# Optimization experiments

Hardware: AMD Instinct MI355X
Metric: run time of the kernel (lower is better)

Reference implementation:

```python
import jax, jax.numpy as jnp
import numpy as np

B, DIM, Hs, Ws = 2, 64, 48, 48
HEADS, DIM_HEAD = 4, 16
INNER = HEADS * DIM_HEAD  # 64
MLP_DIM = 256


def setup_inputs() -> dict:
    key = jax.random.key(0)
    ks = jax.random.split(key, 10)
    w = lambda k, shape: (jax.random.normal(k, shape, jnp.float32) * 0.02)
    return dict(
        x=jax.random.normal(ks[0], (B, DIM, Hs, Ws), jnp.float32),
        y=jax.random.normal(ks[1], (B, DIM, Hs, Ws), jnp.float32),
        ln1_g=jnp.ones((DIM,), jnp.float32), ln1_b=jnp.zeros((DIM,), jnp.float32),
        w_sa1=w(ks[2], (DIM, INNER)), w_sa2=w(ks[3], (DIM, INNER)),
        w_se1=w(ks[4], (DIM, INNER)), w_se2=w(ks[5], (DIM, INNER)),
        w_out=w(ks[6], (INNER, DIM)), b_out=jnp.zeros((DIM,), jnp.float32),
        ln2_g=jnp.ones((DIM,), jnp.float32), ln2_b=jnp.zeros((DIM,), jnp.float32),
        w1=w(ks[7], (DIM, MLP_DIM)), b1=jnp.zeros((MLP_DIM,), jnp.float32),
        w2=w(ks[8], (MLP_DIM, DIM)), b2=jnp.zeros((DIM,), jnp.float32),
    )


def _layer_norm(t, g, b, eps=1e-5):
    m = t.mean(-1, keepdims=True)
    v = t.var(-1, keepdims=True)
    return (t - m) * jax.lax.rsqrt(v + eps) * g + b


def reference(x, y, ln1_g, ln1_b, w_sa1, w_sa2, w_se1, w_se2, w_out, b_out,
              ln2_g, ln2_b, w1, b1, w2, b2):
    b, c, h, wdt = x.shape
    xt = x.reshape(b, c, h * wdt).transpose(0, 2, 1)  # B n C
    yt = y.reshape(b, c, h * wdt).transpose(0, 2, 1)
    n = xt.shape[1]
    scale = DIM_HEAD ** (-0.5)

    # PreNorm: same LayerNorm applied to both x and y (shared params)
    xn = _layer_norm(xt, ln1_g, ln1_b)
    yn = _layer_norm(yt, ln1_g, ln1_b)

    def split_heads(t, wm):  # B n C -> B h n d
        return (t @ wm).reshape(b, n, HEADS, DIM_HEAD).transpose(0, 2, 1, 3)

    y1 = split_heads(yn, w_sa1)
    y2 = split_heads(yn, w_sa2)
    x1 = split_heads(xn, w_se1)
    x2 = split_heads(xn, w_se2)

    # spatial attention map: n x n from y branch
    sacm = jax.nn.softmax(jnp.einsum('bhid,bhjd->bhij', y1, y2) * scale, axis=-1)
    # channel attention map: d x d from x branch
    secm = jax.nn.softmax(jnp.einsum('bhni,bhnj->bhij', x1, x2) * scale / (n / DIM_HEAD), axis=-1)

    out1 = jnp.einsum('bhij,bhjd->bhid', sacm, x1)  # spatial map applied to x values
    out2 = jnp.einsum('bhni,bhij->bhnj', y1, secm)  # channel map applied to y values
    out = (out1 * out2).transpose(0, 2, 1, 3).reshape(b, n, INNER)
    xt = xt + out @ w_out + b_out  # residual around attention

    # MLP with PreNorm + residual, LeakyReLU slope 0.01 (torch default)
    xn2 = _layer_norm(xt, ln2_g, ln2_b)
    hid = jax.nn.leaky_relu(xn2 @ w1 + b1, negative_slope=0.01)
    xt = xt + hid @ w2 + b2

    return xt.transpose(0, 2, 1).reshape(b, c, h, wdt)
```

## Files before the change

### kernel.cpp

```cpp
#include <hip/hip_runtime.h>

#define HW 2304
#define CH 64
typedef unsigned short ushort_t;
typedef __attribute__((ext_vector_type(8))) short bf16x8;
typedef __attribute__((ext_vector_type(4))) float f32x4;

#define QSCL (0.25f * 1.44269504088896340736f)
#define SECM_SCL (0.25f / 144.f)
#define MFMA(a, b, c) __builtin_amdgcn_mfma_f32_16x16x32_bf16((a), (b), (c), 0, 0, 0)

static __device__ __forceinline__ ushort_t f2bf(float f) {
    union { float f; unsigned u; } v; v.f = f;
    unsigned r = v.u + 0x7FFFu + ((v.u >> 16) & 1u);
    return (ushort_t)(r >> 16);
}
static __device__ __forceinline__ unsigned cvtpk(float a, float b) {
    unsigned r;
    asm("v_cvt_pk_bf16_f32 %0, %1, %2" : "=v"(r) : "v"(a), "v"(b));
    return r;
}
union U8 { unsigned u[4]; bf16x8 v; };

__global__ __launch_bounds__(256) void k_wconv(
    const float* __restrict__ wsa1, const float* __restrict__ wsa2,
    const float* __restrict__ wse1, const float* __restrict__ wse2,
    const float* __restrict__ w_out, const float* __restrict__ w1,
    const float* __restrict__ w2,
    ushort_t* __restrict__ wsa1T, ushort_t* __restrict__ wsa2T,
    ushort_t* __restrict__ wse1T, ushort_t* __restrict__ wse2T,
    ushort_t* __restrict__ w_outT, ushort_t* __restrict__ wT1, ushort_t* __restrict__ wT2,
    float* __restrict__ sacc)
{
    const int blk = blockIdx.x, tid = threadIdx.x;
    if (blk < 8) sacc[blk * 256 + tid] = 0.f;
    if (blk < 80) {
        const int mi = blk >> 4;
        const float* s = mi == 0 ? wsa1 : mi == 1 ? wsa2 : mi == 2 ? wse1 : mi == 3 ? wse2 : w_out;
        ushort_t* d = mi == 0 ? wsa1T : mi == 1 ? wsa2T : mi == 2 ? wse1T : mi == 3 ? wse2T : w_outT;
        const int o = (blk & 15) * 256 + tid;
        d[o] = f2bf(s[(o & 63) * 64 + (o >> 6)]);
    } else if (blk < 144) {
        const int o = (blk - 80) * 256 + tid;
        wT1[o] = f2bf(w1[(o & 63) * 256 + (o >> 6)]);
    } else {
        const int o = (blk - 144) * 256 + tid;
        wT2[o] = f2bf(w2[(o & 255) * 64 + (o >> 8)]);
    }
}

__global__ __launch_bounds__(64) void k_ln_proj(
    const float* __restrict__ x, const float* __restrict__ y,
    const float* __restrict__ g, const float* __restrict__ bb,
    const ushort_t* __restrict__ wsa1T, const ushort_t* __restrict__ wsa2T,
    const ushort_t* __restrict__ wse1T, const ushort_t* __restrict__ wse2T,
    float* __restrict__ y1f, ushort_t* __restrict__ qbf, ushort_t* __restrict__ kbf,
    ushort_t* __restrict__ vtbf, float* __restrict__ sacc)
{
    __shared__ ushort_t ldsA[16 * 24 + 32];
    __shared__ ushort_t ldsB[16 * 24 + 32];
    const int task = blockIdx.x;
    const int jt = blockIdx.y;
    const int rt = task % 144;
    const int b  = (task / 144) & 1;
    const int branch = task / 288;
    const int lane = threadIdx.x;
    const int r = lane & 15, cg = lane >> 4;
    const int q0 = rt * 16;
    const float* in = (branch ? y : x) + (size_t)b * CH * HW + q0 + r;
    float lo[8], hi[8];
    float s = 0.f, sq = 0.f;
    #pragma unroll
    for (int ki = 0; ki < 8; ++ki) {
        lo[ki] = in[(size_t)(8 * cg + ki) * HW];
        hi[ki] = in[(size_t)(32 + 8 * cg + ki) * HW];
        s += lo[ki] + hi[ki];
        sq += lo[ki] * lo[ki] + hi[ki] * hi[ki];
    }
    s  += __shfl_xor(s, 16);  s  += __shfl_xor(s, 32);
    sq += __shfl_xor(sq, 16); sq += __shfl_xor(sq, 32);
    const float m  = s * (1.f / 64.f);
    const float rs = rsqrtf(sq * (1.f / 64.f) - m * m + 1e-5f);
    float ga[16], be[16];
    {
        const float4* gp = (const float4*)g;
        const float4* bp = (const float4*)bb;
        *(float4*)&ga[0]  = gp[2 * cg];     *(float4*)&ga[4]  = gp[2 * cg + 1];
        *(float4*)&ga[8]  = gp[8 + 2 * cg]; *(float4*)&ga[12] = gp[9 + 2 * cg];
        *(float4*)&be[0]  = bp[2 * cg];     *(float4*)&be[4]  = bp[2 * cg + 1];
        *(float4*)&be[8]  = bp[8 + 2 * cg]; *(float4*)&be[12] = bp[9 + 2 * cg];
    }
    float nlo[8], nhi[8];
    #pragma unroll
    for (int ki = 0; ki < 8; ++ki) {
        nlo[ki] = (lo[ki] - m) * rs * ga[ki]     + be[ki];
        nhi[ki] = (hi[ki] - m) * rs * ga[8 + ki] + be[8 + ki];
    }
    U8 alo, ahi;
    #pragma unroll
    for (int p = 0; p < 4; ++p) {
        alo.u[p] = cvtpk(nlo[2 * p], nlo[2 * p + 1]);
        ahi.u[p] = cvtpk(nhi[2 * p], nhi[2 * p + 1]);
    }
    const ushort_t* wp1 = branch ? wsa1T : wse1T;
    const ushort_t* wp2 = branch ? wsa2T : wse2T;
    const f32x4 zero4 = {0.f, 0.f, 0.f, 0.f};
    const int bh = b * 4 + jt;
    bf16x8 bl1 = *(const bf16x8*)(wp1 + (jt * 16 + r) * 64 + 8 * cg);
    bf16x8 bh1 = *(const bf16x8*)(wp1 + (jt * 16 + r) * 64 + 32 + 8 * cg);
    f32x4 acc1 = zero4;
    acc1 = MFMA(alo.v, bl1, acc1);
    acc1 = MFMA(ahi.v, bh1, acc1);
    bf16x8 bl2 = *(const bf16x8*)(wp2 + (jt * 16 + r) * 64 + 8 * cg);
    bf16x8 bh2 = *(const bf16x8*)(wp2 + (jt * 16 + r) * 64 + 32 + 8 * cg);
    f32x4 acc2 = zero4;
    acc2 = MFMA(alo.v, bl2, acc2);
    acc2 = MFMA(ahi.v, bh2, acc2);
    if (branch == 0) {
        uint2 pk1; pk1.x = cvtpk(acc1[0], acc1[1]); pk1.y = cvtpk(acc1[2], acc1[3]);
        *(uint2*)(vtbf + (size_t)(bh * 16 + r) * HW + q0 + 4 * cg) = pk1;
        *(uint2*)&ldsA[r * 24 + 4 * cg] = pk1;
        uint2 pk2; pk2.x = cvtpk(acc2[0], acc2[1]); pk2.y = cvtpk(acc2[2], acc2[3]);
        *(uint2*)&ldsB[r * 24 + 4 * cg] = pk2;
        bf16x8 af = {0, 0, 0, 0, 0, 0, 0, 0};
        bf16x8 bf_ = {0, 0, 0, 0, 0, 0, 0, 0};
        if (cg < 2) {
            af  = *(const bf16x8*)&ldsA[r * 24 + 8 * cg];
            bf_ = *(const bf16x8*)&ldsB[r * 24 + 8 * cg];
        }
        f32x4 sp = MFMA(af, bf_, zero4);
        #pragma unroll
        for (int ri = 0; ri < 4; ++ri)
            atomicAdd(&sacc[bh * 256 + (4 * cg + ri) * 16 + r], sp[ri]);
    } else {
        #pragma unroll
        for (int ri = 0; ri < 4; ++ri) {
            const int q = q0 + 4 * cg + ri;
            y1f[((size_t)bh * HW + q) * 16 + r] = acc1[ri];
            qbf[((size_t)bh * HW + q) * 16 + r] = f2bf(acc1[ri] * QSCL);
            kbf[((size_t)bh * HW + q) * 16 + r] = f2bf(acc2[ri]);
        }
    }
}

__global__ __launch_bounds__(512) void k_attn(
    const ushort_t* __restrict__ qbf, const ushort_t* __restrict__ kbf,
    const ushort_t* __restrict__ vtbf, const float* __restrict__ y1f,
    const float* __restrict__ sacc, ushort_t* __restrict__ obf)
{
    __shared__ uint4 pbuf4[8][80];
    __shared__ f32x4 cacc[8][64];
    __shared__ float clsum[8][64];
    __shared__ float sraw[256];
    __shared__ float smv[256];
    const int qt = blockIdx.x, bh = blockIdx.y;
    const int tid = threadIdx.x;
    const int w = tid >> 6, lane = tid & 63;
    const int q16 = lane & 15, g = lane >> 4;
    const int q0 = qt * 16;
    if (tid < 256) sraw[tid] = sacc[bh * 256 + tid] * SECM_SCL;
    __syncthreads();
    if (tid < 256) {
        const int i = tid >> 4;
        float mx = -1e30f;
        #pragma unroll
        for (int jj = 0; jj < 16; ++jj) mx = fmaxf(mx, sraw[i * 16 + jj]);
        float sum = 0.f;
        #pragma unroll
        for (int jj = 0; jj < 16; ++jj) sum += __expf(sraw[i * 16 + jj] - mx);
        smv[tid] = __expf(sraw[tid] - mx) / sum;
    }

    bf16x8 qfrag = {0, 0, 0, 0, 0, 0, 0, 0};
    if (g < 2) qfrag = *(const bf16x8*)(qbf + ((size_t)bh * HW + q0 + q16) * 16 + g * 8);

    unsigned char* pw = (unsigned char*)&pbuf4[w][0];
    const ushort_t* kbase = kbf + (size_t)bh * HW * 16;
    const ushort_t* vbase = vtbf + (size_t)(bh * 16 + q16) * HW;
    f32x4 oacc = {0.f, 0.f, 0.f, 0.f};
    float lsum = 0.f;
    const f32x4 zero4 = {0.f, 0.f, 0.f, 0.f};

    #pragma unroll 3
    for (int wi = 0; wi < 9; ++wi) {
        const int k0 = w * 288 + wi * 32;
        bf16x8 kf0 = *(const bf16x8*)(kbase + (size_t)(k0 + q16) * 16 + (g & 1) * 8);
        bf16x8 kf1 = *(const bf16x8*)(kbase + (size_t)(k0 + 16 + q16) * 16 + (g & 1) * 8);
        f32x4 s0 = MFMA(kf0, qfrag, zero4);
        f32x4 s1 = MFMA(kf1, qfrag, zero4);
        const float e00 = exp2f(s0[0]), e01 = exp2f(s0[1]), e02 = exp2f(s0[2]), e03 = exp2f(s0[3]);
        const float e10 = exp2f(s1[0]), e11 = exp2f(s1[1]), e12 = exp2f(s1[2]), e13 = exp2f(s1[3]);
        lsum += ((e00 + e01) + (e02 + e03)) + ((e10 + e11) + (e12 + e13));
        *(unsigned*)(pw + q16 * 80 + 8 * g)      = cvtpk(e00, e01);
        *(unsigned*)(pw + q16 * 80 + 8 * g + 4)  = cvtpk(e02, e03);
        *(unsigned*)(pw + q16 * 80 + 32 + 8 * g) = cvtpk(e10, e11);
        *(unsigned*)(pw + q16 * 80 + 36 + 8 * g) = cvtpk(e12, e13);
        bf16x8 vfrag = *(const bf16x8*)(vbase + k0 + 8 * g);
        bf16x8 pfrag = *(const bf16x8*)(pw + q16 * 80 + 16 * g);
        oacc = MFMA(vfrag, pfrag, oacc);
    }
    cacc[w][lane] = oacc;
    clsum[w][lane] = lsum;
    __syncthreads();
    if (tid < 64) {
        f32x4 t = cacc[0][lane];
        float L = clsum[0][lane];
        #pragma unroll
        for (int ww = 1; ww < 8; ++ww) {
            f32x4 tw = cacc[ww][lane];
            t[0] += tw[0]; t[1] += tw[1]; t[2] += tw[2]; t[3] += tw[3];
            L += clsum[ww][lane];
        }
        L += __shfl_xor(L, 16);
        L += __shfl_xor(L, 32);
        const float invl = 1.f / L;
        const float* yrow = y1f + ((size_t)bh * HW + q0 + q16) * 16;
        float ya[16];
        #pragma unroll
        for (int i = 0; i < 4; ++i) *(float4*)&ya[4 * i] = ((const float4*)yrow)[i];
        float gate[4] = {0.f, 0.f, 0.f, 0.f};
        #pragma unroll
        for (int i = 0; i < 16; ++i) {
            #pragma unroll
            for (int rr = 0; rr < 4; ++rr) gate[rr] += ya[i] * smv[i * 16 + g * 4 + rr];
        }
        const int b = bh >> 2, h = bh & 3;
        float r0 = t[0] * invl * gate[0];
        float r1 = t[1] * invl * gate[1];
        float r2 = t[2] * invl * gate[2];
        float r3 = t[3] * invl * gate[3];
        uint2 pk; pk.x = cvtpk(r0, r1); pk.y = cvtpk(r2, r3);
        *(uint2*)(obf + ((size_t)b * HW + q0 + q16) * 64 + h * 16 + g * 4) = pk;
    }
}

__global__ __launch_bounds__(256) void k_tail(
    const ushort_t* __restrict__ obf, const float* __restrict__ x,
    const ushort_t* __restrict__ w_outT, const float* __restrict__ b_out,
    const float* __restrict__ g2, const float* __restrict__ bt2,
    const ushort_t* __restrict__ wT1, const float* __restrict__ b1,
    const ushort_t* __restrict__ wT2, const float* __restrict__ b2,
    float* __restrict__ out)
{
    __shared__ float xtile[16][68];
    __shared__ ushort_t hh[16 * 264 + 16];
    const int t = blockIdx.x;
    const int b = t / 144;
    const int q0 = (t % 144) * 16;
    const int tid = threadIdx.x;
    const int w = tid >> 6, lane = tid & 63;
    const int r = lane & 15, cg = lane >> 4;
    const f32x4 zero4 = {0.f, 0.f, 0.f, 0.f};
    const ushort_t* arow = obf + ((size_t)b * HW + q0 + r) * 64;
    bf16x8 alo = *(const bf16x8*)(arow + 8 * cg);
    bf16x8 ahi = *(const bf16x8*)(arow + 32 + 8 * cg);
    {
        bf16x8 bl = *(const bf16x8*)(w_outT + (w * 16 + r) * 64 + 8 * cg);
        bf16x8 bh_ = *(const bf16x8*)(w_outT + (w * 16 + r) * 64 + 32 + 8 * cg);
        f32x4 acc = zero4;
        acc = MFMA(alo, bl, acc);
        acc = MFMA(ahi, bh_, acc);
        const int c = w * 16 + r;
        const float bo = b_out[c];
        float4 xr = *(const float4*)(x + (size_t)b * CH * HW + (size_t)c * HW + q0 + 4 * cg);
        xtile[4 * cg + 0][c] = acc[0] + bo + xr.x;
        xtile[4 * cg + 1][c] = acc[1] + bo + xr.y;
        xtile[4 * cg + 2][c] = acc[2] + bo + xr.z;
        xtile[4 * cg + 3][c] = acc[3] + bo + xr.w;
    }
    __syncthreads();
    float s = 0.f, sq = 0.f;
    #pragma unroll
    for (int j = 0; j < 16; ++j) {
        const float v = xtile[r][cg * 16 + j];
        s += v; sq += v * v;
    }
    s  += __shfl_xor(s, 16);  s  += __shfl_xor(s, 32);
    sq += __shfl_xor(sq, 16); sq += __shfl_xor(sq, 32);
    const float m  = s * (1.f / 64.f);
    const float rs = rsqrtf(sq * (1.f / 64.f) - m * m + 1e-5f);
    float ga[16], be[16];
    {
        const float4* gp = (const float4*)g2;
        const float4* bp = (const float4*)bt2;
        *(float4*)&ga[0]  = gp[2 * cg];     *(float4*)&ga[4]  = gp[2 * cg + 1];
        *(float4*)&ga[8]  = gp[8 + 2 * cg]; *(float4*)&ga[12] = gp[9 + 2 * cg];
        *(float4*)&be[0]  = bp[2 * cg];     *(float4*)&be[4]  = bp[2 * cg + 1];
        *(float4*)&be[8]  = bp[8 + 2 * cg]; *(float4*)&be[12] = bp[9 + 2 * cg];
    }
    float nlo[8], nhi[8];
    #pragma unroll
    for (int ki = 0; ki < 8; ++ki) {
        nlo[ki] = (xtile[r][8 * cg + ki]      - m) * rs * ga[ki]     + be[ki];
        nhi[ki] = (xtile[r][32 + 8 * cg + ki] - m) * rs * ga[8 + ki] + be[8 + ki];
    }
    U8 axlo, axhi;
    #pragma unroll
    for (int p = 0; p < 4; ++p) {
        axlo.u[p] = cvtpk(nlo[2 * p], nlo[2 * p + 1]);
        axhi.u[p] = cvtpk(nhi[2 * p], nhi[2 * p + 1]);
    }
    #pragma unroll
    for (int jj = 0; jj < 4; ++jj) {
        const int jt = 4 * w + jj;
        bf16x8 bl = *(const bf16x8*)(wT1 + (jt * 16 + r) * 64 + 8 * cg);
        bf16x8 bh_ = *(const bf16x8*)(wT1 + (jt * 16 + r) * 64 + 32 + 8 * cg);
        f32x4 acc = zero4;
        acc = MFMA(axlo.v, bl, acc);
        acc = MFMA(axhi.v, bh_, acc);
        const int c = jt * 16 + r;
        const float bias = b1[c];
        #pragma unroll
        for (int ri = 0; ri < 4; ++ri) {
            float vv = acc[ri] + bias;
            vv = fmaxf(vv, 0.01f * vv);
            hh[(4 * cg + ri) * 264 + c] = f2bf(vv);
        }
    }
    __syncthreads();
    bf16x8 ha[8];
    #pragma unroll
    for (int kw = 0; kw < 8; ++kw)
        ha[kw] = *(const bf16x8*)&hh[r * 264 + kw * 32 + 8 * cg];
    f32x4 acc = zero4;
    #pragma unroll
    for (int kw = 0; kw < 8; ++kw) {
        bf16x8 bf_ = *(const bf16x8*)(wT2 + (w * 16 + r) * 256 + kw * 32 + 8 * cg);
        acc = MFMA(ha[kw], bf_, acc);
    }
    const int c = w * 16 + r;
    const float bias = b2[c];
    float4 res;
    res.x = acc[0] + bias + xtile[4 * cg + 0][c];
    res.y = acc[1] + bias + xtile[4 * cg + 1][c];
    res.z = acc[2] + bias + xtile[4 * cg + 2][c];
    res.w = acc[3] + bias + xtile[4 * cg + 3][c];
    *(float4*)(out + (size_t)b * CH * HW + (size_t)c * HW + q0 + 4 * cg) = res;
}

extern "C" void kernel_launch(void* const* d_in, const int* in_sizes, int n_in,
                              void* d_out, int out_size, void* d_ws, size_t ws_size,
                              hipStream_t stream)
{
    (void)in_sizes; (void)n_in; (void)out_size; (void)ws_size;
    const float* x     = (const float*)d_in[0];
    const float* y     = (const float*)d_in[1];
    const float* ln1_g = (const float*)d_in[2];
    const float* ln1_b = (const float*)d_in[3];
    const float* w_sa1 = (const float*)d_in[4];
    const float* w_sa2 = (const float*)d_in[5];
    const float* w_se1 = (const float*)d_in[6];
    const float* w_se2 = (const float*)d_in[7];
    const float* w_out = (const float*)d_in[8];
    const float* b_out = (const float*)d_in[9];
    const float* ln2_g = (const float*)d_in[10];
    const float* ln2_b = (const float*)d_in[11];
    const float* w1    = (const float*)d_in[12];
    const float* b1    = (const float*)d_in[13];
    const float* w2    = (const float*)d_in[14];
    const float* b2    = (const float*)d_in[15];
    float* out = (float*)d_out;

    const size_t NP = 8ull * HW * 16;
    float* p = (float*)d_ws;
    float* y1f  = p;  p += NP;
    float* sacc = p;  p += 2048;
    ushort_t* u = (ushort_t*)p;
    ushort_t* qbf   = u;  u += NP;
    ushort_t* kbf   = u;  u += NP;
    ushort_t* vtbf  = u;  u += NP;
    ushort_t* obf   = u;  u += NP;
    ushort_t* wsa1T = u;  u += 4096;
    ushort_t* wsa2T = u;  u += 4096;
    ushort_t* wse1T = u;  u += 4096;
    ushort_t* wse2T = u;  u += 4096;
    ushort_t* w_outT= u;  u += 4096;
    ushort_t* wT1   = u;  u += 16384;
    ushort_t* wT2   = u;  u += 16384;

    k_wconv<<<208, 256, 0, stream>>>(w_sa1, w_sa2, w_se1, w_se2, w_out, w1, w2,
                                     wsa1T, wsa2T, wse1T, wse2T, w_outT, wT1, wT2,
                                     sacc);
    k_ln_proj<<<dim3(576, 4), 64, 0, stream>>>(x, y, ln1_g, ln1_b,
                                               wsa1T, wsa2T, wse1T, wse2T,
                                               y1f, qbf, kbf, vtbf, sacc);
    k_attn<<<dim3(144, 8), 512, 0, stream>>>(qbf, kbf, vtbf, y1f, sacc, obf);
    k_tail<<<288, 256, 0, stream>>>(obf, x, w_outT, b_out, ln2_g, ln2_b,
                                    wT1, b1, wT2, b2, out);
}
```

Measured before the change: 119.3 us.

## Fuse all stages into one persistent kernel with software grid barriers

Replaces the four separate launches (weight conversion, LN+projection, attention, tail MLP) with a small init kernel plus one persistent kernel of 768 blocks that runs each stage in turn, separated by atomic-counter grid barriers. Stages share a union of LDS buffers, and work is redistributed across 256-thread blocks, with the attention stage using 4 waves instead of 8. The aim is to remove per-launch overhead and the gaps between dependent kernels. In exchange it relies on all 768 blocks being co-resident (launch bounds request 3 blocks per CU), which risks deadlock or spin overhead. The attention parallelism per block is also reduced.

```diff
diff --git a/kernel.cpp b/kernel.cpp
--- a/kernel.cpp
+++ b/kernel.cpp
@@ -2,6 +2,7 @@
 
 #define HW 2304
 #define CH 64
+#define NBLK 768
 typedef unsigned short ushort_t;
 typedef __attribute__((ext_vector_type(8))) short bf16x8;
 typedef __attribute__((ext_vector_type(4))) float f32x4;
@@ -22,320 +23,337 @@
 }
 union U8 { unsigned u[4]; bf16x8 v; };
 
-__global__ __launch_bounds__(256) void k_wconv(
+__global__ __launch_bounds__(256) void k_init(int* __restrict__ bar, float* __restrict__ sacc)
+{
+    const int tid = threadIdx.x;
+    if (tid < 16) bar[tid] = 0;
+    #pragma unroll
+    for (int i = 0; i < 8; ++i) sacc[i * 256 + tid] = 0.f;
+}
+
+static __device__ __forceinline__ void gridbar(int* bar, int phase)
+{
+    __syncthreads();
+    if (threadIdx.x == 0) {
+        int prev = __hip_atomic_fetch_add(&bar[0], 1, __ATOMIC_ACQ_REL, __HIP_MEMORY_SCOPE_AGENT);
+        if (prev == NBLK - 1) {
+            __hip_atomic_store(&bar[0], 0, __ATOMIC_RELAXED, __HIP_MEMORY_SCOPE_AGENT);
+            __hip_atomic_store(&bar[1], phase, __ATOMIC_RELEASE, __HIP_MEMORY_SCOPE_AGENT);
+        } else {
+            while (__hip_atomic_load(&bar[1], __ATOMIC_ACQUIRE, __HIP_MEMORY_SCOPE_AGENT) < phase)
+                __builtin_amdgcn_s_sleep(1);
+        }
+    }
+    __syncthreads();
+}
+
+__global__ __launch_bounds__(256, 3) void k_mega(
+    const float* __restrict__ x, const float* __restrict__ y,
+    const float* __restrict__ ln1g, const float* __restrict__ ln1b,
     const float* __restrict__ wsa1, const float* __restrict__ wsa2,
     const float* __restrict__ wse1, const float* __restrict__ wse2,
-    const float* __restrict__ w_out, const float* __restrict__ w1,
-    const float* __restrict__ w2,
+    const float* __restrict__ w_out, const float* __restrict__ b_out,
+    const float* __restrict__ ln2g, const float* __restrict__ ln2b,
+    const float* __restrict__ w1, const float* __restrict__ mb1,
+    const float* __restrict__ w2, const float* __restrict__ mb2,
+    float* __restrict__ y1f, float* __restrict__ sacc, int* __restrict__ bar,
+    ushort_t* __restrict__ qbf, ushort_t* __restrict__ kbf,
+    ushort_t* __restrict__ vtbf, ushort_t* __restrict__ obf,
     ushort_t* __restrict__ wsa1T, ushort_t* __restrict__ wsa2T,
     ushort_t* __restrict__ wse1T, ushort_t* __restrict__ wse2T,
     ushort_t* __restrict__ w_outT, ushort_t* __restrict__ wT1, ushort_t* __restrict__ wT2,
-    float* __restrict__ sacc)
-{
-    const int blk = blockIdx.x, tid = threadIdx.x;
-    if (blk < 8) sacc[blk * 256 + tid] = 0.f;
-    if (blk < 80) {
-        const int mi = blk >> 4;
-        const float* s = mi == 0 ? wsa1 : mi == 1 ? wsa2 : mi == 2 ? wse1 : mi == 3 ? wse2 : w_out;
-        ushort_t* d = mi == 0 ? wsa1T : mi == 1 ? wsa2T : mi == 2 ? wse1T : mi == 3 ? wse2T : w_outT;
-        const int o = (blk & 15) * 256 + tid;
-        d[o] = f2bf(s[(o & 63) * 64 + (o >> 6)]);
-    } else if (blk < 144) {
-        const int o = (blk - 80) * 256 + tid;
-        wT1[o] = f2bf(w1[(o & 63) * 256 + (o >> 6)]);
-    } else {
-        const int o = (blk - 144) * 256 + tid;
-        wT2[o] = f2bf(w2[(o & 255) * 64 + (o >> 8)]);
-    }
-}
-
-__global__ __launch_bounds__(64) void k_ln_proj(
-    const float* __restrict__ x, const float* __restrict__ y,
-    const float* __restrict__ g, const float* __restrict__ bb,
-    const ushort_t* __restrict__ wsa1T, const ushort_t* __restrict__ wsa2T,
-    const ushort_t* __restrict__ wse1T, const ushort_t* __restrict__ wse2T,
-    float* __restrict__ y1f, ushort_t* __restrict__ qbf, ushort_t* __restrict__ kbf,
-    ushort_t* __restrict__ vtbf, float* __restrict__ sacc)
-{
-    __shared__ ushort_t ldsA[16 * 24 + 32];
-    __shared__ ushort_t ldsB[16 * 24 + 32];
-    const int task = blockIdx.x;
-    const int jt = blockIdx.y;
-    const int rt = task % 144;
-    const int b  = (task / 144) & 1;
-    const int branch = task / 288;
-    const int lane = threadIdx.x;
-    const int r = lane & 15, cg = lane >> 4;
-    const int q0 = rt * 16;
-    const float* in = (branch ? y : x) + (size_t)b * CH * HW + q0 + r;
-    float lo[8], hi[8];
-    float s = 0.f, sq = 0.f;
-    #pragma unroll
-    for (int ki = 0; ki < 8; ++ki) {
-        lo[ki] = in[(size_t)(8 * cg + ki) * HW];
-        hi[ki] = in[(size_t)(32 + 8 * cg + ki) * HW];
-        s += lo[ki] + hi[ki];
-        sq += lo[ki] * lo[ki] + hi[ki] * hi[ki];
-    }
-    s  += __shfl_xor(s, 16);  s  += __shfl_xor(s, 32);
-    sq += __shfl_xor(sq, 16); sq += __shfl_xor(sq, 32);
-    const float m  = s * (1.f / 64.f);
-    const float rs = rsqrtf(sq * (1.f / 64.f) - m * m + 1e-5f);
-    float ga[16], be[16];
-    {
-        const float4* gp = (const float4*)g;
-        const float4* bp = (const float4*)bb;
-        *(float4*)&ga[0]  = gp[2 * cg];     *(float4*)&ga[4]  = gp[2 * cg + 1];
-        *(float4*)&ga[8]  = gp[8 + 2 * cg]; *(float4*)&ga[12] = gp[9 + 2 * cg];
-        *(float4*)&be[0]  = bp[2 * cg];     *(float4*)&be[4]  = bp[2 * cg + 1];
-        *(float4*)&be[8]  = bp[8 + 2 * cg]; *(float4*)&be[12] = bp[9 + 2 * cg];
-    }
-    float nlo[8], nhi[8];
-    #pragma unroll
-    for (int ki = 0; ki < 8; ++ki) {
-        nlo[ki] = (lo[ki] - m) * rs * ga[ki]     + be[ki];
-        nhi[ki] = (hi[ki] - m) * rs * ga[8 + ki] + be[8 + ki];
-    }
-    U8 alo, ahi;
-    #pragma unroll
-    for (int p = 0; p < 4; ++p) {
-        alo.u[p] = cvtpk(nlo[2 * p], nlo[2 * p + 1]);
-        ahi.u[p] = cvtpk(nhi[2 * p], nhi[2 * p + 1]);
-    }
-    const ushort_t* wp1 = branch ? wsa1T : wse1T;
-    const ushort_t* wp2 = branch ? wsa2T : wse2T;
-    const f32x4 zero4 = {0.f, 0.f, 0.f, 0.f};
-    const int bh = b * 4 + jt;
-    bf16x8 bl1 = *(const bf16x8*)(wp1 + (jt * 16 + r) * 64 + 8 * cg);
-    bf16x8 bh1 = *(const bf16x8*)(wp1 + (jt * 16 + r) * 64 + 32 + 8 * cg);
-    f32x4 acc1 = zero4;
-    acc1 = MFMA(alo.v, bl1, acc1);
-    acc1 = MFMA(ahi.v, bh1, acc1);
-    bf16x8 bl2 = *(const bf16x8*)(wp2 + (jt * 16 + r) * 64 + 8 * cg);
-    bf16x8 bh2 = *(const bf16x8*)(wp2 + (jt * 16 + r) * 64 + 32 + 8 * cg);
-    f32x4 acc2 = zero4;
-    acc2 = MFMA(alo.v, bl2, acc2);
-    acc2 = MFMA(ahi.v, bh2, acc2);
-    if (branch == 0) {
-        uint2 pk1; pk1.x = cvtpk(acc1[0], acc1[1]); pk1.y = cvtpk(acc1[2], acc1[3]);
-        *(uint2*)(vtbf + (size_t)(bh * 16 + r) * HW + q0 + 4 * cg) = pk1;
-        *(uint2*)&ldsA[r * 24 + 4 * cg] = pk1;
-        uint2 pk2; pk2.x = cvtpk(acc2[0], acc2[1]); pk2.y = cvtpk(acc2[2], acc2[3]);
-        *(uint2*)&ldsB[r * 24 + 4 * cg] = pk2;
-        bf16x8 af = {0, 0, 0, 0, 0, 0, 0, 0};
-        bf16x8 bf_ = {0, 0, 0, 0, 0, 0, 0, 0};
-        if (cg < 2) {
-            af  = *(const bf16x8*)&ldsA[r * 24 + 8 * cg];
-            bf_ = *(const bf16x8*)&ldsB[r * 24 + 8 * cg];
-        }
-        f32x4 sp = MFMA(af, bf_, zero4);
-        #pragma unroll
-        for (int ri = 0; ri < 4; ++ri)
-            atomicAdd(&sacc[bh * 256 + (4 * cg + ri) * 16 + r], sp[ri]);
-    } else {
-        #pragma unroll
-        for (int ri = 0; ri < 4; ++ri) {
-            const int q = q0 + 4 * cg + ri;
-            y1f[((size_t)bh * HW + q) * 16 + r] = acc1[ri];
-            qbf[((size_t)bh * HW + q) * 16 + r] = f2bf(acc1[ri] * QSCL);
-            kbf[((size_t)bh * HW + q) * 16 + r] = f2bf(acc2[ri]);
-        }
-    }
-}
-
-__global__ __launch_bounds__(512) void k_attn(
-    const ushort_t* __restrict__ qbf, const ushort_t* __restrict__ kbf,
-    const ushort_t* __restrict__ vtbf, const float* __restrict__ y1f,
-    const float* __restrict__ sacc, ushort_t* __restrict__ obf)
-{
-    __shared__ uint4 pbuf4[8][80];
-    __shared__ f32x4 cacc[8][64];
-    __shared__ float clsum[8][64];
-    __shared__ float sraw[256];
-    __shared__ float smv[256];
-    const int qt = blockIdx.x, bh = blockIdx.y;
-    const int tid = threadIdx.x;
-    const int w = tid >> 6, lane = tid & 63;
-    const int q16 = lane & 15, g = lane >> 4;
-    const int q0 = qt * 16;
-    if (tid < 256) sraw[tid] = sacc[bh * 256 + tid] * SECM_SCL;
-    __syncthreads();
-    if (tid < 256) {
-        const int i = tid >> 4;
-        float mx = -1e30f;
-        #pragma unroll
-        for (int jj = 0; jj < 16; ++jj) mx = fmaxf(mx, sraw[i * 16 + jj]);
-        float sum = 0.f;
-        #pragma unroll
-        for (int jj = 0; jj < 16; ++jj) sum += __expf(sraw[i * 16 + jj] - mx);
-        smv[tid] = __expf(sraw[tid] - mx) / sum;
-    }
-
-    bf16x8 qfrag = {0, 0, 0, 0, 0, 0, 0, 0};
-    if (g < 2) qfrag = *(const bf16x8*)(qbf + ((size_t)bh * HW + q0 + q16) * 16 + g * 8);
-
-    unsigned char* pw = (unsigned char*)&pbuf4[w][0];
-    const ushort_t* kbase = kbf + (size_t)bh * HW * 16;
-    const ushort_t* vbase = vtbf + (size_t)(bh * 16 + q16) * HW;
-    f32x4 oacc = {0.f, 0.f, 0.f, 0.f};
-    float lsum = 0.f;
-    const f32x4 zero4 = {0.f, 0.f, 0.f, 0.f};
-
-    #pragma unroll 3
-    for (int wi = 0; wi < 9; ++wi) {
-        const int k0 = w * 288 + wi * 32;
-        bf16x8 kf0 = *(const bf16x8*)(kbase + (size_t)(k0 + q16) * 16 + (g & 1) * 8);
-        bf16x8 kf1 = *(const bf16x8*)(kbase + (size_t)(k0 + 16 + q16) * 16 + (g & 1) * 8);
-        f32x4 s0 = MFMA(kf0, qfrag, zero4);
-        f32x4 s1 = MFMA(kf1, qfrag, zero4);
-        const float e00 = exp2f(s0[0]), e01 = exp2f(s0[1]), e02 = exp2f(s0[2]), e03 = exp2f(s0[3]);
-        const float e10 = exp2f(s1[0]), e11 = exp2f(s1[1]), e12 = exp2f(s1[2]), e13 = exp2f(s1[3]);
-        lsum += ((e00 + e01) + (e02 + e03)) + ((e10 + e11) + (e12 + e13));
-        *(unsigned*)(pw + q16 * 80 + 8 * g)      = cvtpk(e00, e01);
-        *(unsigned*)(pw + q16 * 80 + 8 * g + 4)  = cvtpk(e02, e03);
-        *(unsigned*)(pw + q16 * 80 + 32 + 8 * g) = cvtpk(e10, e11);
-        *(unsigned*)(pw + q16 * 80 + 36 + 8 * g) = cvtpk(e12, e13);
-        bf16x8 vfrag = *(const bf16x8*)(vbase + k0 + 8 * g);
-        bf16x8 pfrag = *(const bf16x8*)(pw + q16 * 80 + 16 * g);
-        oacc = MFMA(vfrag, pfrag, oacc);
-    }
-    cacc[w][lane] = oacc;
-    clsum[w][lane] = lsum;
-    __syncthreads();
-    if (tid < 64) {
-        f32x4 t = cacc[0][lane];
-        float L = clsum[0][lane];
-        #pragma unroll
-        for (int ww = 1; ww < 8; ++ww) {
-            f32x4 tw = cacc[ww][lane];
-            t[0] += tw[0]; t[1] += tw[1]; t[2] += tw[2]; t[3] += tw[3];
-            L += clsum[ww][lane];
-        }
-        L += __shfl_xor(L, 16);
-        L += __shfl_xor(L, 32);
-        const float invl = 1.f / L;
-        const float* yrow = y1f + ((size_t)bh * HW + q0 + q16) * 16;
-        float ya[16];
-        #pragma unroll
-        for (int i = 0; i < 4; ++i) *(float4*)&ya[4 * i] = ((const float4*)yrow)[i];
-        float gate[4] = {0.f, 0.f, 0.f, 0.f};
-        #pragma unroll
-        for (int i = 0; i < 16; ++i) {
-            #pragma unroll
-            for (int rr = 0; rr < 4; ++rr) gate[rr] += ya[i] * smv[i * 16 + g * 4 + rr];
-        }
-        const int b = bh >> 2, h = bh & 3;
-        float r0 = t[0] * invl * gate[0];
-        float r1 = t[1] * invl * gate[1];
-        float r2 = t[2] * invl * gate[2];
-        float r3 = t[3] * invl * gate[3];
-        uint2 pk; pk.x = cvtpk(r0, r1); pk.y = cvtpk(r2, r3);
-        *(uint2*)(obf + ((size_t)b * HW + q0 + q16) * 64 + h * 16 + g * 4) = pk;
-    }
-}
-
-__global__ __launch_bounds__(256) void k_tail(
-    const ushort_t* __restrict__ obf, const float* __restrict__ x,
-    const ushort_t* __restrict__ w_outT, const float* __restrict__ b_out,
-    const float* __restrict__ g2, const float* __restrict__ bt2,
-    const ushort_t* __restrict__ wT1, const float* __restrict__ b1,
-    const ushort_t* __restrict__ wT2, const float* __restrict__ b2,
     float* __restrict__ out)
 {
-    __shared__ float xtile[16][68];
-    __shared__ ushort_t hh[16 * 264 + 16];
-    const int t = blockIdx.x;
-    const int b = t / 144;
-    const int q0 = (t % 144) * 16;
-    const int tid = threadIdx.x;
-    const int w = tid >> 6, lane = tid & 63;
-    const int r = lane & 15, cg = lane >> 4;
+    union SM {
+        struct { uint4 pbuf4[4][80]; f32x4 cacc[4][64]; float clsum[4][64];
+                 float sraw[256]; float smv[256]; } a;
+        struct { float xtile[16][68]; ushort_t hh[16 * 264 + 16]; } t;
+        struct { ushort_t A[4][416]; ushort_t B[4][416]; } l;
+    };
+    __shared__ SM sm;
     const f32x4 zero4 = {0.f, 0.f, 0.f, 0.f};
-    const ushort_t* arow = obf + ((size_t)b * HW + q0 + r) * 64;
-    bf16x8 alo = *(const bf16x8*)(arow + 8 * cg);
-    bf16x8 ahi = *(const bf16x8*)(arow + 32 + 8 * cg);
+
     {
-        bf16x8 bl = *(const bf16x8*)(w_outT + (w * 16 + r) * 64 + 8 * cg);
-        bf16x8 bh_ = *(const bf16x8*)(w_outT + (w * 16 + r) * 64 + 32 + 8 * cg);
+        const int idx = blockIdx.x * 256 + threadIdx.x;
+        if (idx < 20480) {
+            const int mi = idx >> 12, o = idx & 4095;
+            const float* s = mi == 0 ? wsa1 : mi == 1 ? wsa2 : mi == 2 ? wse1 : mi == 3 ? wse2 : w_out;
+            ushort_t* d = mi == 0 ? wsa1T : mi == 1 ? wsa2T : mi == 2 ? wse1T : mi == 3 ? wse2T : w_outT;
+            d[o] = f2bf(s[(o & 63) * 64 + (o >> 6)]);
+        } else if (idx < 36864) {
+            const int o = idx - 20480;
+            wT1[o] = f2bf(w1[(o & 63) * 256 + (o >> 6)]);
+        } else if (idx < 53248) {
+            const int o = idx - 36864;
+            wT2[o] = f2bf(w2[(o & 255) * 64 + (o >> 8)]);
+        }
+    }
+    gridbar(bar, 1);
+
+    {
+        const int tid = threadIdx.x;
+        const int w = tid >> 6, lane = tid & 63;
+        const int task = blockIdx.x + w * NBLK;
+        if (task < 2304) {
+            const int jt = task / 576;
+            const int t576 = task % 576;
+            const int rt = t576 % 144;
+            const int b  = (t576 / 144) & 1;
+            const int branch = t576 / 288;
+            const int r = lane & 15, cg = lane >> 4;
+            const int q0 = rt * 16;
+            const float* xin = (branch ? y : x) + (size_t)b * CH * HW + q0 + r;
+            float lo[8], hi[8];
+            float s = 0.f, sq = 0.f;
+            #pragma unroll
+            for (int ki = 0; ki < 8; ++ki) {
+                lo[ki] = xin[(size_t)(8 * cg + ki) * HW];
+                hi[ki] = xin[(size_t)(32 + 8 * cg + ki) * HW];
+                s += lo[ki] + hi[ki];
+                sq += lo[ki] * lo[ki] + hi[ki] * hi[ki];
+            }
+            s  += __shfl_xor(s, 16);  s  += __shfl_xor(s, 32);
+            sq += __shfl_xor(sq, 16); sq += __shfl_xor(sq, 32);
+            const float m  = s * (1.f / 64.f);
+            const float rs = rsqrtf(sq * (1.f / 64.f) - m * m + 1e-5f);
+            float ga[16], be[16];
+            {
+                const float4* gp = (const float4*)ln1g;
+                const float4* bp = (const float4*)ln1b;
+                *(float4*)&ga[0]  = gp[2 * cg];     *(float4*)&ga[4]  = gp[2 * cg + 1];
+                *(float4*)&ga[8]  = gp[8 + 2 * cg]; *(float4*)&ga[12] = gp[9 + 2 * cg];
+                *(float4*)&be[0]  = bp[2 * cg];     *(float4*)&be[4]  = bp[2 * cg + 1];
+                *(float4*)&be[8]  = bp[8 + 2 * cg]; *(float4*)&be[12] = bp[9 + 2 * cg];
+            }
+            float nlo[8], nhi[8];
+            #pragma unroll
+            for (int ki = 0; ki < 8; ++ki) {
+                nlo[ki] = (lo[ki] - m) * rs * ga[ki]     + be[ki];
+                nhi[ki] = (hi[ki] - m) * rs * ga[8 + ki] + be[8 + ki];
+            }
+            U8 alo, ahi;
+            #pragma unroll
+            for (int p = 0; p < 4; ++p) {
+                alo.u[p] = cvtpk(nlo[2 * p], nlo[2 * p + 1]);
+                ahi.u[p] = cvtpk(nhi[2 * p], nhi[2 * p + 1]);
+            }
+            const ushort_t* wp1 = branch ? wsa1T : wse1T;
+            const ushort_t* wp2 = branch ? wsa2T : wse2T;
+            const int bh = b * 4 + jt;
+            bf16x8 bl1 = *(const bf16x8*)(wp1 + (jt * 16 + r) * 64 + 8 * cg);
+            bf16x8 bh1 = *(const bf16x8*)(wp1 + (jt * 16 + r) * 64 + 32 + 8 * cg);
+            f32x4 acc1 = zero4;
+            acc1 = MFMA(alo.v, bl1, acc1);
+            acc1 = MFMA(ahi.v, bh1, acc1);
+            bf16x8 bl2 = *(const bf16x8*)(wp2 + (jt * 16 + r) * 64 + 8 * cg);
+            bf16x8 bh2 = *(const bf16x8*)(wp2 + (jt * 16 + r) * 64 + 32 + 8 * cg);
+            f32x4 acc2 = zero4;
+            acc2 = MFMA(alo.v, bl2, acc2);
+            acc2 = MFMA(ahi.v, bh2, acc2);
+            if (branch == 0) {
+                uint2 pk1; pk1.x = cvtpk(acc1[0], acc1[1]); pk1.y = cvtpk(acc1[2], acc1[3]);
+                *(uint2*)(vtbf + (size_t)(bh * 16 + r) * HW + q0 + 4 * cg) = pk1;
+                *(uint2*)&sm.l.A[w][r * 24 + 4 * cg] = pk1;
+                uint2 pk2; pk2.x = cvtpk(acc2[0], acc2[1]); pk2.y = cvtpk(acc2[2], acc2[3]);
+                *(uint2*)&sm.l.B[w][r * 24 + 4 * cg] = pk2;
+                bf16x8 af = {0, 0, 0, 0, 0, 0, 0, 0};
+                bf16x8 bf_ = {0, 0, 0, 0, 0, 0, 0, 0};
+                if (cg < 2) {
+                    af  = *(const bf16x8*)&sm.l.A[w][r * 24 + 8 * cg];
+                    bf_ = *(const bf16x8*)&sm.l.B[w][r * 24 + 8 * cg];
+                }
+                f32x4 sp = MFMA(af, bf_, zero4);
+                #pragma unroll
+                for (int ri = 0; ri < 4; ++ri)
+                    atomicAdd(&sacc[bh * 256 + (4 * cg + ri) * 16 + r], sp[ri]);
+            } else {
+                #pragma unroll
+                for (int ri = 0; ri < 4; ++ri) {
+                    const int q = q0 + 4 * cg + ri;
+                    y1f[((size_t)bh * HW + q) * 16 + r] = acc1[ri];
+                    qbf[((size_t)bh * HW + q) * 16 + r] = f2bf(acc1[ri] * QSCL);
+                    kbf[((size_t)bh * HW + q) * 16 + r] = f2bf(acc2[ri]);
+                }
+            }
+        }
+    }
+    gridbar(bar, 2);
+
+    {
+        const int tid = threadIdx.x;
+        const int w = tid >> 6, lane = tid & 63;
+        const int q16 = lane & 15, g = lane >> 4;
+        unsigned char* pw = (unsigned char*)&sm.a.pbuf4[w][0];
+        for (int t = blockIdx.x; t < 1152; t += NBLK) {
+            const int qt = t % 144, bh = t / 144;
+            const int q0 = qt * 16;
+            sm.a.sraw[tid] = sacc[bh * 256 + tid] * SECM_SCL;
+            __syncthreads();
+            {
+                const int i = tid >> 4;
+                float mx = -1e30f;
+                #pragma unroll
+                for (int jj = 0; jj < 16; ++jj) mx = fmaxf(mx, sm.a.sraw[i * 16 + jj]);
+                float sum = 0.f;
+                #pragma unroll
+                for (int jj = 0; jj < 16; ++jj) sum += __expf(sm.a.sraw[i * 16 + jj] - mx);
+                sm.a.smv[tid] = __expf(sm.a.sraw[tid] - mx) / sum;
+            }
+            bf16x8 qfrag = {0, 0, 0, 0, 0, 0, 0, 0};
+            if (g < 2) qfrag = *(const bf16x8*)(qbf + ((size_t)bh * HW + q0 + q16) * 16 + g * 8);
+            const ushort_t* kbase = kbf + (size_t)bh * HW * 16;
+            const ushort_t* vbase = vtbf + (size_t)(bh * 16 + q16) * HW;
+            f32x4 oacc = zero4;
+            float lsum = 0.f;
+            #pragma unroll 2
+            for (int wi = 0; wi < 18; ++wi) {
+                const int k0 = w * 576 + wi * 32;
+                bf16x8 kf0 = *(const bf16x8*)(kbase + (size_t)(k0 + q16) * 16 + (g & 1) * 8);
+                bf16x8 kf1 = *(const bf16x8*)(kbase + (size_t)(k0 + 16 + q16) * 16 + (g & 1) * 8);
+                f32x4 s0 = MFMA(kf0, qfrag, zero4);
+                f32x4 s1 = MFMA(kf1, qfrag, zero4);
+                const float e00 = exp2f(s0[0]), e01 = exp2f(s0[1]), e02 = exp2f(s0[2]), e03 = exp2f(s0[3]);
+                const float e10 = exp2f(s1[0]), e11 = exp2f(s1[1]), e12 = exp2f(s1[2]), e13 = exp2f(s1[3]);
+                lsum += ((e00 + e01) + (e02 + e03)) + ((e10 + e11) + (e12 + e13));
+                *(unsigned*)(pw + q16 * 80 + 8 * g)      = cvtpk(e00, e01);
+                *(unsigned*)(pw + q16 * 80 + 8 * g + 4)  = cvtpk(e02, e03);
+                *(unsigned*)(pw + q16 * 80 + 32 + 8 * g) = cvtpk(e10, e11);
+                *(unsigned*)(pw + q16 * 80 + 36 + 8 * g) = cvtpk(e12, e13);
+                bf16x8 vfrag = *(const bf16x8*)(vbase + k0 + 8 * g);
+                bf16x8 pfrag = *(const bf16x8*)(pw + q16 * 80 + 16 * g);
+                oacc = MFMA(vfrag, pfrag, oacc);
+            }
+            sm.a.cacc[w][lane] = oacc;
+            sm.a.clsum[w][lane] = lsum;
+            __syncthreads();
+            if (tid < 64) {
+                f32x4 tt = sm.a.cacc[0][lane];
+                float L = sm.a.clsum[0][lane];
+                #pragma unroll
+                for (int ww = 1; ww < 4; ++ww) {
+                    f32x4 tw = sm.a.cacc[ww][lane];
+                    tt[0] += tw[0]; tt[1] += tw[1]; tt[2] += tw[2]; tt[3] += tw[3];
+                    L += sm.a.clsum[ww][lane];
+                }
+                L += __shfl_xor(L, 16);
+                L += __shfl_xor(L, 32);
+                const float invl = 1.f / L;
+                const float* yrow = y1f + ((size_t)bh * HW + q0 + q16) * 16;
+                float ya[16];
+                #pragma unroll
+                for (int i = 0; i < 4; ++i) *(float4*)&ya[4 * i] = ((const float4*)yrow)[i];
+                float gate[4] = {0.f, 0.f, 0.f, 0.f};
+                #pragma unroll
+                for (int i = 0; i < 16; ++i) {
+                    #pragma unroll
+                    for (int rr = 0; rr < 4; ++rr) gate[rr] += ya[i] * sm.a.smv[i * 16 + g * 4 + rr];
+                }
+                const int b = bh >> 2, h = bh & 3;
+                float r0 = tt[0] * invl * gate[0];
+                float r1 = tt[1] * invl * gate[1];
+                float r2 = tt[2] * invl * gate[2];
+                float r3 = tt[3] * invl * gate[3];
+                uint2 pk; pk.x = cvtpk(r0, r1); pk.y = cvtpk(r2, r3);
+                *(uint2*)(obf + ((size_t)b * HW + q0 + q16) * 64 + h * 16 + g * 4) = pk;
+            }
+            __syncthreads();
+        }
+    }
+    gridbar(bar, 3);
+
+    if (blockIdx.x < 288) {
+        const int t = blockIdx.x;
+        const int b = t / 144;
+        const int q0 = (t % 144) * 16;
+        const int tid = threadIdx.x;
+        const int w = tid >> 6, lane = tid & 63;
+        const int r = lane & 15, cg = lane >> 4;
+        const ushort_t* arow = obf + ((size_t)b * HW + q0 + r) * 64;
+        bf16x8 alo = *(const bf16x8*)(arow + 8 * cg);
+        bf16x8 ahi = *(const bf16x8*)(arow + 32 + 8 * cg);
+        {
+            bf16x8 bl = *(const bf16x8*)(w_outT + (w * 16 + r) * 64 + 8 * cg);
+            bf16x8 bh_ = *(const bf16x8*)(w_outT + (w * 16 + r) * 64 + 32 + 8 * cg);
+            f32x4 acc = zero4;
+            acc = MFMA(alo, bl, acc);
+            acc = MFMA(ahi, bh_, acc);
+            const int c = w * 16 + r;
+            const float bo = b_out[c];
+            float4 xr = *(const float4*)(x + (size_t)b * CH * HW + (size_t)c * HW + q0 + 4 * cg);
+            sm.t.xtile[4 * cg + 0][c] = acc[0] + bo + xr.x;
+            sm.t.xtile[4 * cg + 1][c] = acc[1] + bo + xr.y;
+            sm.t.xtile[4 * cg + 2][c] = acc[2] + bo + xr.z;
+            sm.t.xtile[4 * cg + 3][c] = acc[3] + bo + xr.w;
+        }
+        __syncthreads();
+        float s = 0.f, sq = 0.f;
+        #pragma unroll
+        for (int j = 0; j < 16; ++j) {
+            const float v = sm.t.xtile[r][cg * 16 + j];
+            s += v; sq += v * v;
+        }
+        s  += __shfl_xor(s, 16);  s  += __shfl_xor(s, 32);
+        sq += __shfl_xor(sq, 16); sq += __shfl_xor(sq, 32);
+        const float m  = s * (1.f / 64.f);
+        const float rs = rsqrtf(sq * (1.f / 64.f) - m * m + 1e-5f);
+        float ga[16], be[16];
+        {
+            const float4* gp = (const float4*)ln2g;
+            const float4* bp = (const float4*)ln2b;
+            *(float4*)&ga[0]  = gp[2 * cg];     *(float4*)&ga[4]  = gp[2 * cg + 1];
+            *(float4*)&ga[8]  = gp[8 + 2 * cg]; *(float4*)&ga[12] = gp[9 + 2 * cg];
+            *(float4*)&be[0]  = bp[2 * cg];     *(float4*)&be[4]  = bp[2 * cg + 1];
+            *(float4*)&be[8]  = bp[8 + 2 * cg]; *(float4*)&be[12] = bp[9 + 2 * cg];
+        }
+        float nlo[8], nhi[8];
+        #pragma unroll
+        for (int ki = 0; ki < 8; ++ki) {
+            nlo[ki] = (sm.t.xtile[r][8 * cg + ki]      - m) * rs * ga[ki]     + be[ki];
+            nhi[ki] = (sm.t.xtile[r][32 + 8 * cg + ki] - m) * rs * ga[8 + ki] + be[8 + ki];
+        }
+        U8 axlo, axhi;
+        #pragma unroll
+        for (int p = 0; p < 4; ++p) {
+            axlo.u[p] = cvtpk(nlo[2 * p], nlo[2 * p + 1]);
+            axhi.u[p] = cvtpk(nhi[2 * p], nhi[2 * p + 1]);
+        }
+        #pragma unroll
+        for (int jj = 0; jj < 4; ++jj) {
+            const int jt = 4 * w + jj;
+            bf16x8 bl = *(const bf16x8*)(wT1 + (jt * 16 + r) * 64 + 8 * cg);
+            bf16x8 bh_ = *(const bf16x8*)(wT1 + (jt * 16 + r) * 64 + 32 + 8 * cg);
+            f32x4 acc = zero4;
+            acc = MFMA(axlo.v, bl, acc);
+            acc = MFMA(axhi.v, bh_, acc);
+            const int c = jt * 16 + r;
+            const float bias = mb1[c];
+            #pragma unroll
+            for (int ri = 0; ri < 4; ++ri) {
+                float vv = acc[ri] + bias;
+                vv = fmaxf(vv, 0.01f * vv);
+                sm.t.hh[(4 * cg + ri) * 264 + c] = f2bf(vv);
+            }
+        }
+        __syncthreads();
+        bf16x8 ha[8];
+        #pragma unroll
+        for (int kw = 0; kw < 8; ++kw)
+            ha[kw] = *(const bf16x8*)&sm.t.hh[r * 264 + kw * 32 + 8 * cg];
         f32x4 acc = zero4;
-        acc = MFMA(alo, bl, acc);
-        acc = MFMA(ahi, bh_, acc);
+        #pragma unroll
+        for (int kw = 0; kw < 8; ++kw) {
+            bf16x8 bf_ = *(const bf16x8*)(wT2 + (w * 16 + r) * 256 + kw * 32 + 8 * cg);
+            acc = MFMA(ha[kw], bf_, acc);
+        }
         const int c = w * 16 + r;
-        const float bo = b_out[c];
-        float4 xr = *(const float4*)(x + (size_t)b * CH * HW + (size_t)c * HW + q0 + 4 * cg);
-        xtile[4 * cg + 0][c] = acc[0] + bo + xr.x;
-        xtile[4 * cg + 1][c] = acc[1] + bo + xr.y;
-        xtile[4 * cg + 2][c] = acc[2] + bo + xr.z;
-        xtile[4 * cg + 3][c] = acc[3] + bo + xr.w;
+        const float bias = mb2[c];
+        float4 res;
+        res.x = acc[0] + bias + sm.t.xtile[4 * cg + 0][c];
+        res.y = acc[1] + bias + sm.t.xtile[4 * cg + 1][c];
+        res.z = acc[2] + bias + sm.t.xtile[4 * cg + 2][c];
+        res.w = acc[3] + bias + sm.t.xtile[4 * cg + 3][c];
+        *(float4*)(out + (size_t)b * CH * HW + (size_t)c * HW + q0 + 4 * cg) = res;
     }
-    __syncthreads();
-    float s = 0.f, sq = 0.f;
-    #pragma unroll
-    for (int j = 0; j < 16; ++j) {
-        const float v = xtile[r][cg * 16 + j];
-        s += v; sq += v * v;
-    }
-    s  += __shfl_xor(s, 16);  s  += __shfl_xor(s, 32);
-    sq += __shfl_xor(sq, 16); sq += __shfl_xor(sq, 32);
-    const float m  = s * (1.f / 64.f);
-    const float rs = rsqrtf(sq * (1.f / 64.f) - m * m + 1e-5f);
-    float ga[16], be[16];
-    {
-        const float4* gp = (const float4*)g2;
-        const float4* bp = (const float4*)bt2;
-        *(float4*)&ga[0]  = gp[2 * cg];     *(float4*)&ga[4]  = gp[2 * cg + 1];
-        *(float4*)&ga[8]  = gp[8 + 2 * cg]; *(float4*)&ga[12] = gp[9 + 2 * cg];
-        *(float4*)&be[0]  = bp[2 * cg];     *(float4*)&be[4]  = bp[2 * cg + 1];
-        *(float4*)&be[8]  = bp[8 + 2 * cg]; *(float4*)&be[12] = bp[9 + 2 * cg];
-    }
-    float nlo[8], nhi[8];
-    #pragma unroll
-    for (int ki = 0; ki < 8; ++ki) {
-        nlo[ki] = (xtile[r][8 * cg + ki]      - m) * rs * ga[ki]     + be[ki];
-        nhi[ki] = (xtile[r][32 + 8 * cg + ki] - m) * rs * ga[8 + ki] + be[8 + ki];
-    }
-    U8 axlo, axhi;
-    #pragma unroll
-    for (int p = 0; p < 4; ++p) {
-        axlo.u[p] = cvtpk(nlo[2 * p], nlo[2 * p + 1]);
-        axhi.u[p] = cvtpk(nhi[2 * p], nhi[2 * p + 1]);
-    }
-    #pragma unroll
-    for (int jj = 0; jj < 4; ++jj) {
-        const int jt = 4 * w + jj;
-        bf16x8 bl = *(const bf16x8*)(wT1 + (jt * 16 + r) * 64 + 8 * cg);
-        bf16x8 bh_ = *(const bf16x8*)(wT1 + (jt * 16 + r) * 64 + 32 + 8 * cg);
-        f32x4 acc = zero4;
-        acc = MFMA(axlo.v, bl, acc);
-        acc = MFMA(axhi.v, bh_, acc);
-        const int c = jt * 16 + r;
-        const float bias = b1[c];
-        #pragma unroll
-        for (int ri = 0; ri < 4; ++ri) {
-            float vv = acc[ri] + bias;
-            vv = fmaxf(vv, 0.01f * vv);
-            hh[(4 * cg + ri) * 264 + c] = f2bf(vv);
-        }
-    }
-    __syncthreads();
-    bf16x8 ha[8];
-    #pragma unroll
-    for (int kw = 0; kw < 8; ++kw)
-        ha[kw] = *(const bf16x8*)&hh[r * 264 + kw * 32 + 8 * cg];
-    f32x4 acc = zero4;
-    #pragma unroll
-    for (int kw = 0; kw < 8; ++kw) {
-        bf16x8 bf_ = *(const bf16x8*)(wT2 + (w * 16 + r) * 256 + kw * 32 + 8 * cg);
-        acc = MFMA(ha[kw], bf_, acc);
-    }
-    const int c = w * 16 + r;
-    const float bias = b2[c];
-    float4 res;
-    res.x = acc[0] + bias + xtile[4 * cg + 0][c];
-    res.y = acc[1] + bias + xtile[4 * cg + 1][c];
-    res.z = acc[2] + bias + xtile[4 * cg + 2][c];
-    res.w = acc[3] + bias + xtile[4 * cg + 3][c];
-    *(float4*)(out + (size_t)b * CH * HW + (size_t)c * HW + q0 + 4 * cg) = res;
 }
 
 extern "C" void kernel_launch(void* const* d_in, const int* in_sizes, int n_in,
@@ -365,6 +383,7 @@
     float* p = (float*)d_ws;
     float* y1f  = p;  p += NP;
     float* sacc = p;  p += 2048;
+    int*   bar  = (int*)p;  p += 16;
     ushort_t* u = (ushort_t*)p;
     ushort_t* qbf   = u;  u += NP;
     ushort_t* kbf   = u;  u += NP;
@@ -378,13 +397,14 @@
     ushort_t* wT1   = u;  u += 16384;
     ushort_t* wT2   = u;  u += 16384;
 
-    k_wconv<<<208, 256, 0, stream>>>(w_sa1, w_sa2, w_se1, w_se2, w_out, w1, w2,
-                                     wsa1T, wsa2T, wse1T, wse2T, w_outT, wT1, wT2,
-                                     sacc);
-    k_ln_proj<<<dim3(576, 4), 64, 0, stream>>>(x, y, ln1_g, ln1_b,
-                                               wsa1T, wsa2T, wse1T, wse2T,
-                                               y1f, qbf, kbf, vtbf, sacc);
-    k_attn<<<dim3(144, 8), 512, 0, stream>>>(qbf, kbf, vtbf, y1f, sacc, obf);
-    k_tail<<<288, 256, 0, stream>>>(obf, x, w_outT, b_out, ln2_g, ln2_b,
-                                    wT1, b1, wT2, b2, out);
-}
+    k_init<<<1, 256, 0, stream>>>(bar, sacc);
+    k_mega<<<NBLK, 256, 0, stream>>>(x, y, ln1_g, ln1_b,
+                                     w_sa1, w_sa2, w_se1, w_se2,
+                                     w_out, b_out, ln2_g, ln2_b,
+                                     w1, b1, w2, b2,
+                                     y1f, sacc, bar,
+                                     qbf, kbf, vtbf, obf,
+                                     wsa1T, wsa2T, wse1T, wse2T,
+                                     w_outT, wT1, wT2,
+                                     out);
+}
```

Result: slower. 358.8 us (+200.7%).
